# Performance work log

Hardware: AMD Instinct MI355X
Metric: run time of the kernel (lower is better)

The kernel has to match this reference:

```python
import jax, jax.numpy as jnp
import numpy as np

N, E, IN, H, OUT = 100000, 600000, 128, 128, 64
BN_EPS = 1e-5


def setup_inputs() -> dict:
    key = jax.random.key(0)
    ks = jax.random.split(key, 8)
    def lin(k, i, o):
        return jax.random.normal(k, (i, o), jnp.float32) / np.float32(np.sqrt(i))
    return {
        "x": jax.random.normal(ks[0], (N, IN), jnp.float32),
        "edge_index": jax.random.randint(ks[1], (2, E), 0, N, dtype=jnp.int64),
        "W1": lin(ks[2], IN, H), "b1": jnp.zeros((H,), jnp.float32),
        "gamma": jnp.ones((H,), jnp.float32), "beta": jnp.zeros((H,), jnp.float32),
        "W2": lin(ks[3], H, H), "b2": jnp.zeros((H,), jnp.float32),
        "Wm1": lin(ks[4], H, H), "bm1": jnp.zeros((H,), jnp.float32),
        "Wm2": lin(ks[5], H, OUT), "bm2": jnp.zeros((OUT,), jnp.float32),
    }


def reference(x, edge_index, W1, b1, gamma, beta, W2, b2, Wm1, bm1, Wm2, bm2):
    # GINConv: h = MLP((1 + eps) * x + sum_{j in N(i)} x_j), eps = 0 (train_eps=False)
    src = edge_index[0]
    dst = edge_index[1]  # PyG aggregates messages at edge_index[1]
    agg = jax.ops.segment_sum(x[src], dst, num_segments=x.shape[0])  # [N, IN]
    h = agg + x
    # inner MLP: Linear -> BatchNorm (batch stats) -> ReLU -> Linear
    h = h @ W1 + b1
    mean = jnp.mean(h, axis=0)
    var = jnp.var(h, axis=0)
    h = (h - mean) * jax.lax.rsqrt(var + BN_EPS) * gamma + beta
    h = jax.nn.relu(h)
    h = h @ W2 + b2
    h = jax.nn.relu(h)  # .relu() after conv
    # output MLP (norm=None, dropout=0.5 -> identity at inference): Linear -> ReLU -> Linear
    h = jax.nn.relu(h @ Wm1 + bm1)
    return h @ Wm2 + bm2
```

## Files before the change

### kernel.cpp

```cpp
#include <hip/hip_runtime.h>
#include <hip/hip_bf16.h>
#include <stdint.h>

#define NNODES 100000
#define NEDGES 600000
#define SCAN_CHUNK 1024
#define SCAN_NB 98

typedef __attribute__((ext_vector_type(8))) short bf16x8;
typedef __attribute__((ext_vector_type(4))) float f32x4;
typedef __attribute__((ext_vector_type(4))) unsigned int u32x4;

__device__ inline float b2f(short b) {
    union { unsigned u; float f; } v;
    v.u = ((unsigned)(unsigned short)b) << 16;
    return v.f;
}
__device__ inline short f2b(float f) {
    union { float f; unsigned u; } v;
    v.f = f;
    unsigned r = (v.u + 0x7FFFu + ((v.u >> 16) & 1u)) >> 16;
    return (short)r;
}
__device__ inline unsigned packbf(float lo, float hi) {
    return ((unsigned)(unsigned short)f2b(hi) << 16) | (unsigned)(unsigned short)f2b(lo);
}
#define MFMA16(a, b, c) __builtin_amdgcn_mfma_f32_16x16x32_bf16(a, b, c, 0, 0, 0)

__global__ __launch_bounds__(256) void k_prep(const float* __restrict__ x,
                                              const float* __restrict__ W1,
                                              const float* __restrict__ W2,
                                              const float* __restrict__ Wm1,
                                              const float* __restrict__ Wm2,
                                              short* __restrict__ xb, short* __restrict__ Wt,
                                              int* __restrict__ pos, float* __restrict__ stats) {
    int i = blockIdx.x * 256 + threadIdx.x;
    if (i < (NNODES + 1) * 16) {
        bf16x8 o = (bf16x8){0, 0, 0, 0, 0, 0, 0, 0};
        if (i < NNODES * 16) {
            const float4* p = (const float4*)(x + (size_t)i * 8);
            float4 a = p[0], b = p[1];
            o[0] = f2b(a.x); o[1] = f2b(a.y); o[2] = f2b(a.z); o[3] = f2b(a.w);
            o[4] = f2b(b.x); o[5] = f2b(b.y); o[6] = f2b(b.z); o[7] = f2b(b.w);
        }
        *(bf16x8*)(xb + (size_t)i * 8) = o;
    }
    if (i < NNODES) pos[i] = 0;
    if (i < 57344) {
        int jj, lane, kt, ct;
        const float* W;
        int ldw, off;
        if (i < 16384) { off = i; W = W1; ldw = 128; }
        else if (i < 32768) { off = i - 16384; W = W2; ldw = 128; }
        else if (i < 49152) { off = i - 32768; W = Wm1; ldw = 128; }
        else { off = i - 49152; W = Wm2; ldw = 64; }
        jj = off & 7;
        lane = (off >> 3) & 63;
        kt = (off >> 9) & 3;
        ct = (off >> 11) & 7;
        int lr = lane & 15, hi = lane >> 4;
        int c = ct * 16 + lr;
        int k = kt * 32 + hi * 8 + jj;
        Wt[i] = f2b(W[k * ldw + c]);
    }
    if (i < 256) stats[i] = 0.0f;
}


__global__ __launch_bounds__(256) void k_hist(const int* __restrict__ ei, int* __restrict__ cnt) {
    int e = blockIdx.x * 256 + threadIdx.x;
    if (e < NEDGES) atomicAdd(&cnt[ei[NEDGES + e]], 1);
}

__global__ __launch_bounds__(256) void k_scan1(const int* __restrict__ cnt, int* __restrict__ bsums) {
    __shared__ int sd[256];
    int b = blockIdx.x, t = threadIdx.x;
    int base = b * SCAN_CHUNK + t * 4;
    int s = 0;
#pragma unroll
    for (int i = 0; i < 4; ++i) {
        int idx = base + i;
        if (idx < NNODES) s += cnt[idx];
    }
    sd[t] = s;
    __syncthreads();
    for (int off = 128; off > 0; off >>= 1) {
        if (t < off) sd[t] += sd[t + off];
        __syncthreads();
    }
    if (t == 0) bsums[b] = sd[0];
}

__global__ __launch_bounds__(64) void k_scan2(int* __restrict__ bsums, int* __restrict__ rowptr) {
    if (threadIdx.x == 0 && blockIdx.x == 0) {
        int run = 0;
        for (int b = 0; b < SCAN_NB; ++b) {
            int v = bsums[b];
            bsums[b] = run;
            run += v;
        }
        rowptr[NNODES] = run;
    }
}

__global__ __launch_bounds__(256) void k_scan3(const int* __restrict__ cnt,
                                               const int* __restrict__ bsums,
                                               int* __restrict__ rowptr, int* __restrict__ pos) {
    __shared__ int sd[256];
    int b = blockIdx.x, t = threadIdx.x;
    int base = b * SCAN_CHUNK + t * 4;
    int v[4];
    int s = 0;
#pragma unroll
    for (int i = 0; i < 4; ++i) {
        int idx = base + i;
        v[i] = (idx < NNODES) ? cnt[idx] : 0;
        s += v[i];
    }
    sd[t] = s;
    __syncthreads();
    for (int off = 1; off < 256; off <<= 1) {
        int val = (t >= off) ? sd[t - off] : 0;
        __syncthreads();
        sd[t] += val;
        __syncthreads();
    }
    int run = sd[t] - s + bsums[b];
#pragma unroll
    for (int i = 0; i < 4; ++i) {
        int idx = base + i;
        if (idx < NNODES) {
            rowptr[idx] = run;
            pos[idx] = run;
            run += v[i];
        }
    }
}

__global__ __launch_bounds__(256) void k_fill(const int* __restrict__ ei, int* __restrict__ pos,
                                              int* __restrict__ elist) {
    int e = blockIdx.x * 256 + threadIdx.x;
    if (e >= NEDGES) return;
    int src = ei[e];
    int dst = ei[NEDGES + e];
    int p = atomicAdd(&pos[dst], 1);
    elist[p] = src;
}

__global__ __launch_bounds__(256) void k_agg(const short* __restrict__ xb,
                                             const int* __restrict__ rowptr,
                                             const int* __restrict__ elist,
                                             short* __restrict__ bufb) {
    int t = threadIdx.x;
    int w = t >> 6, lane = t & 63;
    int node = blockIdx.x * 4 + w;
    if (node >= NNODES) return;
    int beg = rowptr[node];
    int end = rowptr[node + 1];
    int deg = end - beg;
    int total = deg + 1;
    int sub = lane & 31, half = lane >> 5;
    const uint2* xr = (const uint2*)xb;

    float acc0 = 0.f, acc1 = 0.f, acc2 = 0.f, acc3 = 0.f;

    for (int base = 0; base < total; base += 64) {
        int j = base + lane;
        int ej = NNODES;
        if (j < total) ej = (j == 0) ? node : elist[beg + j - 1];
        int cnt = min(64, total - base);
        int pairs = (cnt + 1) >> 1;
        for (int i = 0; i < pairs; i += 4) {
            int j0 = 2 * i + half;
            int r0 = __shfl(ej, j0);
            int r1 = __shfl(ej, j0 + 2);
            int r2 = __shfl(ej, j0 + 4);
            int r3 = __shfl(ej, j0 + 6);
            uint2 v0 = xr[(size_t)r0 * 32 + sub];
            uint2 v1 = xr[(size_t)r1 * 32 + sub];
            uint2 v2 = xr[(size_t)r2 * 32 + sub];
            uint2 v3 = xr[(size_t)r3 * 32 + sub];
            acc0 += b2f((short)(v0.x & 0xFFFF)) + b2f((short)(v1.x & 0xFFFF)) +
                    b2f((short)(v2.x & 0xFFFF)) + b2f((short)(v3.x & 0xFFFF));
            acc1 += b2f((short)(v0.x >> 16)) + b2f((short)(v1.x >> 16)) +
                    b2f((short)(v2.x >> 16)) + b2f((short)(v3.x >> 16));
            acc2 += b2f((short)(v0.y & 0xFFFF)) + b2f((short)(v1.y & 0xFFFF)) +
                    b2f((short)(v2.y & 0xFFFF)) + b2f((short)(v3.y & 0xFFFF));
            acc3 += b2f((short)(v0.y >> 16)) + b2f((short)(v1.y >> 16)) +
                    b2f((short)(v2.y >> 16)) + b2f((short)(v3.y >> 16));
        }
    }
    acc0 += __shfl_xor(acc0, 32);
    acc1 += __shfl_xor(acc1, 32);
    acc2 += __shfl_xor(acc2, 32);
    acc3 += __shfl_xor(acc3, 32);
    if (half == 0) {
        uint2 o;
        o.x = ((uint32_t)(unsigned short)f2b(acc1) << 16) | (uint32_t)(unsigned short)f2b(acc0);
        o.y = ((uint32_t)(unsigned short)f2b(acc3) << 16) | (uint32_t)(unsigned short)f2b(acc2);
        ((uint2*)bufb)[(size_t)node * 32 + sub] = o;
    }
}

__global__ __launch_bounds__(256) void k_stats(const short* __restrict__ bufb,
                                               const short* __restrict__ W1pk,
                                               float* __restrict__ stats) {
    __shared__ float Sred[2][4][128];
    int t = threadIdx.x, w = t >> 6, l = t & 63;
    int r0 = blockIdx.x * 128;
    int row0 = (w & 1) * 64, col0 = (w >> 1) * 64;

    f32x4 acc[4][4];
#pragma unroll
    for (int r = 0; r < 4; ++r)
#pragma unroll
        for (int c = 0; c < 4; ++c) acc[r][c] = (f32x4){0.f, 0.f, 0.f, 0.f};

#pragma unroll
    for (int kb = 0; kb < 4; ++kb) {
        bf16x8 af[4], bw[4];
#pragma unroll
        for (int r = 0; r < 4; ++r)
            af[r] = *(const bf16x8*)(bufb + (size_t)(r0 + row0 + r * 16 + (l & 15)) * 128 +
                                     kb * 32 + (l >> 4) * 8);
#pragma unroll
        for (int c = 0; c < 4; ++c)
            bw[c] = *(const bf16x8*)(W1pk + ((((w >> 1) * 4 + c) * 4 + kb) * 64 + l) * 8);
#pragma unroll
        for (int r = 0; r < 4; ++r)
#pragma unroll
            for (int c = 0; c < 4; ++c) acc[r][c] = MFMA16(af[r], bw[c], acc[r][c]);
    }

    float s[4], q[4];
#pragma unroll
    for (int c = 0; c < 4; ++c) { s[c] = 0.f; q[c] = 0.f; }
#pragma unroll
    for (int c = 0; c < 4; ++c)
#pragma unroll
        for (int r = 0; r < 4; ++r)
#pragma unroll
            for (int rr = 0; rr < 4; ++rr) {
                int grow = r0 + row0 + r * 16 + (l >> 4) * 4 + rr;
                if (grow < NNODES) {
                    float v = acc[r][c][rr];
                    s[c] += v;
                    q[c] += v * v;
                }
            }
#pragma unroll
    for (int c = 0; c < 4; ++c) {
        s[c] += __shfl_xor(s[c], 16); s[c] += __shfl_xor(s[c], 32);
        q[c] += __shfl_xor(q[c], 16); q[c] += __shfl_xor(q[c], 32);
    }
    if (l < 16) {
#pragma unroll
        for (int c = 0; c < 4; ++c) {
            Sred[0][w][col0 + c * 16 + l] = s[c];
            Sred[1][w][col0 + c * 16 + l] = q[c];
        }
    }
    __syncthreads();
    if (t < 128) {
        int wb = (t < 64) ? 0 : 2;
        atomicAdd(stats + t, Sred[0][wb][t] + Sred[0][wb + 1][t]);
        atomicAdd(stats + 128 + t, Sred[1][wb][t] + Sred[1][wb + 1][t]);
    }
}

__global__ __launch_bounds__(256, 4) void k_mlp(const short* __restrict__ bufb,
                                                const float* __restrict__ stats,
                                                const float* __restrict__ gamma,
                                                const float* __restrict__ beta,
                                                const short* __restrict__ Wt,
                                                const float* __restrict__ b2,
                                                const float* __restrict__ bm1,
                                                const float* __restrict__ bm2,
                                                float* __restrict__ out) {
    __shared__ float scale[128], shift[128], b2s[128], bm1s[128], bm2s[64];

    int t = threadIdx.x, w = t >> 6, l = t & 63;
    int lr = l & 15, hi = l >> 4;
    size_t node0 = (size_t)blockIdx.x * 64 + w * 16;
    const short* W1pk = Wt;
    const short* W2pk = Wt + 16384;
    const short* Wm1pk = Wt + 32768;
    const short* Wm2pk = Wt + 49152;

    if (t < 128) {
        float mean = stats[t] * (1.0f / NNODES);
        float var = stats[128 + t] * (1.0f / NNODES) - mean * mean;
        var = fmaxf(var, 0.0f);
        float inv = rsqrtf(var + 1e-5f);
        float sc = gamma[t] * inv;
        scale[t] = sc;
        shift[t] = beta[t] - mean * sc;
        b2s[t] = b2[t];
        bm1s[t] = bm1[t];
    }
    if (t < 64) bm2s[t] = bm2[t];
    __syncthreads();

    bf16x8 bv[4];
#pragma unroll
    for (int kt = 0; kt < 4; ++kt)
        bv[kt] = *(const bf16x8*)(bufb + (node0 + lr) * 128 + kt * 32 + hi * 8);

    unsigned pw[8][2];

#pragma unroll
    for (int ct = 0; ct < 8; ++ct) {
        f32x4 a = (f32x4){0.f, 0.f, 0.f, 0.f};
#pragma unroll
        for (int kt = 0; kt < 4; ++kt)
            a = MFMA16(*(const bf16x8*)(W1pk + ((ct * 4 + kt) * 64 + l) * 8), bv[kt], a);
        int c0 = ct * 16 + hi * 4;
        float4 sc4 = *(const float4*)&scale[c0];
        float4 sh4 = *(const float4*)&shift[c0];
        float v0 = fmaxf(a[0] * sc4.x + sh4.x, 0.f);
        float v1 = fmaxf(a[1] * sc4.y + sh4.y, 0.f);
        float v2 = fmaxf(a[2] * sc4.z + sh4.z, 0.f);
        float v3 = fmaxf(a[3] * sc4.w + sh4.w, 0.f);
        pw[ct][0] = packbf(v0, v1);
        pw[ct][1] = packbf(v2, v3);
    }

#define REDIST()                                                                        \
    {                                                                                   \
        int h2 = hi >> 1, h1 = hi & 1;                                                  \
        _Pragma("unroll") for (int kt = 0; kt < 4; ++kt) {                              \
            unsigned nw[4];                                                             \
            _Pragma("unroll") for (int jp = 0; jp < 4; ++jp) {                          \
                int srcl = (2 * h1 + (jp >> 1)) * 16 + lr;                              \
                unsigned ve = (unsigned)__shfl((int)pw[2 * kt][jp & 1], srcl);          \
                unsigned vo = (unsigned)__shfl((int)pw[2 * kt + 1][jp & 1], srcl);      \
                nw[jp] = h2 ? vo : ve;                                                  \
            }                                                                           \
            u32x4 uq = (u32x4){nw[0], nw[1], nw[2], nw[3]};                             \
            bv[kt] = __builtin_bit_cast(bf16x8, uq);                                    \
        }                                                                               \
    }
    REDIST();

#pragma unroll
    for (int ct = 0; ct < 8; ++ct) {
        f32x4 a = (f32x4){0.f, 0.f, 0.f, 0.f};
#pragma unroll
        for (int kt = 0; kt < 4; ++kt)
            a = MFMA16(*(const bf16x8*)(W2pk + ((ct * 4 + kt) * 64 + l) * 8), bv[kt], a);
        int c0 = ct * 16 + hi * 4;
        float4 bb = *(const float4*)&b2s[c0];
        float v0 = fmaxf(a[0] + bb.x, 0.f);
        float v1 = fmaxf(a[1] + bb.y, 0.f);
        float v2 = fmaxf(a[2] + bb.z, 0.f);
        float v3 = fmaxf(a[3] + bb.w, 0.f);
        pw[ct][0] = packbf(v0, v1);
        pw[ct][1] = packbf(v2, v3);
    }
    REDIST();

#pragma unroll
    for (int ct = 0; ct < 8; ++ct) {
        f32x4 a = (f32x4){0.f, 0.f, 0.f, 0.f};
#pragma unroll
        for (int kt = 0; kt < 4; ++kt)
            a = MFMA16(*(const bf16x8*)(Wm1pk + ((ct * 4 + kt) * 64 + l) * 8), bv[kt], a);
        int c0 = ct * 16 + hi * 4;
        float4 bb = *(const float4*)&bm1s[c0];
        float v0 = fmaxf(a[0] + bb.x, 0.f);
        float v1 = fmaxf(a[1] + bb.y, 0.f);
        float v2 = fmaxf(a[2] + bb.z, 0.f);
        float v3 = fmaxf(a[3] + bb.w, 0.f);
        pw[ct][0] = packbf(v0, v1);
        pw[ct][1] = packbf(v2, v3);
    }
    REDIST();

#pragma unroll
    for (int ct = 0; ct < 4; ++ct) {
        f32x4 a = (f32x4){0.f, 0.f, 0.f, 0.f};
#pragma unroll
        for (int kt = 0; kt < 4; ++kt)
            a = MFMA16(bv[kt], *(const bf16x8*)(Wm2pk + ((ct * 4 + kt) * 64 + l) * 8), a);
        float bias = bm2s[ct * 16 + lr];
#pragma unroll
        for (int rr = 0; rr < 4; ++rr) {
            size_t grow = node0 + hi * 4 + rr;
            if (grow < NNODES) out[grow * 64 + ct * 16 + lr] = a[rr] + bias;
        }
    }
}

extern "C" void kernel_launch(void* const* d_in, const int* in_sizes, int n_in,
                              void* d_out, int out_size, void* d_ws, size_t ws_size,
                              hipStream_t stream) {
    const float* x     = (const float*)d_in[0];
    const int*   ei    = (const int*)d_in[1];
    const float* W1    = (const float*)d_in[2];
    const float* gamma = (const float*)d_in[4];
    const float* beta  = (const float*)d_in[5];
    const float* W2    = (const float*)d_in[6];
    const float* b2    = (const float*)d_in[7];
    const float* Wm1   = (const float*)d_in[8];
    const float* bm1   = (const float*)d_in[9];
    const float* Wm2   = (const float*)d_in[10];
    const float* bm2   = (const float*)d_in[11];
    float* out = (float*)d_out;

    char* ws = (char*)d_ws;
    short* xb    = (short*)ws;
    short* bufb  = xb + (size_t)(NNODES + 1) * 128;
    short* Wt    = bufb + (size_t)(NNODES + 128) * 128;
    float* stats = (float*)(Wt + 57344);
    int* rowptr  = (int*)(stats + 256);
    int* pos     = rowptr + (NNODES + 1);
    int* elist   = pos + NNODES;
    int* bsums   = elist + NEDGES;

    int gE = (NEDGES + 255) / 256;
    int gPrep = ((NNODES + 1) * 16 + 255) / 256;

    k_prep<<<gPrep, 256, 0, stream>>>(x, W1, W2, Wm1, Wm2, xb, Wt, pos, stats);
    k_hist<<<gE, 256, 0, stream>>>(ei, pos);
    k_scan1<<<SCAN_NB, 256, 0, stream>>>(pos, bsums);
    k_scan2<<<1, 64, 0, stream>>>(bsums, rowptr);
    k_scan3<<<SCAN_NB, 256, 0, stream>>>(pos, bsums, rowptr, pos);
    k_fill<<<gE, 256, 0, stream>>>(ei, pos, elist);
    k_agg<<<(NNODES + 3) / 4, 256, 0, stream>>>(xb, rowptr, elist, bufb);

    int nblkS = (NNODES + 127) / 128;
    k_stats<<<nblkS, 256, 0, stream>>>(bufb, Wt, stats);
    int nblkM = (NNODES + 63) / 64;
    k_mlp<<<nblkM, 256, 0, stream>>>(bufb, stats, gamma, beta, Wt, b2, bm1, bm2, out);
}
```

Before: 190.6 us.

## Process two 16-node tiles per wave in MLP kernel to reuse weight loads

Each wave in k_mlp now handles 32 nodes as two 16-row tiles that share every weight fragment load, halving weight traffic per node. The three hidden layers are folded into one loop with per-layer scale/shift tables, and the block count is halved. Register pressure roughly doubles, so launch bounds drop from 4 to 3 blocks per CU, which reduces occupancy. A non-unrolled layer loop may add indexing overhead.

```diff
diff --git a/kernel.cpp b/kernel.cpp
--- a/kernel.cpp
+++ b/kernel.cpp
@@ -268,7 +268,7 @@
     }
 }
 
-__global__ __launch_bounds__(256, 4) void k_mlp(const short* __restrict__ bufb,
+__global__ __launch_bounds__(256, 3) void k_mlp(const short* __restrict__ bufb,
                                                 const float* __restrict__ stats,
                                                 const float* __restrict__ gamma,
                                                 const float* __restrict__ beta,
@@ -277,116 +277,115 @@
                                                 const float* __restrict__ bm1,
                                                 const float* __restrict__ bm2,
                                                 float* __restrict__ out) {
-    __shared__ float scale[128], shift[128], b2s[128], bm1s[128], bm2s[64];
+    __shared__ float scl[3][128], shf[3][128], bm2s[64];
 
     int t = threadIdx.x, w = t >> 6, l = t & 63;
     int lr = l & 15, hi = l >> 4;
-    size_t node0 = (size_t)blockIdx.x * 64 + w * 16;
-    const short* W1pk = Wt;
-    const short* W2pk = Wt + 16384;
-    const short* Wm1pk = Wt + 32768;
+    size_t node0 = (size_t)blockIdx.x * 128 + w * 32;
     const short* Wm2pk = Wt + 49152;
 
     if (t < 128) {
         float mean = stats[t] * (1.0f / NNODES);
-        float var = stats[128 + t] * (1.0f / NNODES) - mean * mean;
-        var = fmaxf(var, 0.0f);
+        float var = fmaxf(stats[128 + t] * (1.0f / NNODES) - mean * mean, 0.0f);
         float inv = rsqrtf(var + 1e-5f);
         float sc = gamma[t] * inv;
-        scale[t] = sc;
-        shift[t] = beta[t] - mean * sc;
-        b2s[t] = b2[t];
-        bm1s[t] = bm1[t];
+        scl[0][t] = sc;
+        shf[0][t] = beta[t] - mean * sc;
+        scl[1][t] = 1.0f;
+        shf[1][t] = b2[t];
+        scl[2][t] = 1.0f;
+        shf[2][t] = bm1[t];
     }
     if (t < 64) bm2s[t] = bm2[t];
     __syncthreads();
 
-    bf16x8 bv[4];
-#pragma unroll
-    for (int kt = 0; kt < 4; ++kt)
-        bv[kt] = *(const bf16x8*)(bufb + (node0 + lr) * 128 + kt * 32 + hi * 8);
-
-    unsigned pw[8][2];
-
-#pragma unroll
-    for (int ct = 0; ct < 8; ++ct) {
-        f32x4 a = (f32x4){0.f, 0.f, 0.f, 0.f};
-#pragma unroll
-        for (int kt = 0; kt < 4; ++kt)
-            a = MFMA16(*(const bf16x8*)(W1pk + ((ct * 4 + kt) * 64 + l) * 8), bv[kt], a);
-        int c0 = ct * 16 + hi * 4;
-        float4 sc4 = *(const float4*)&scale[c0];
-        float4 sh4 = *(const float4*)&shift[c0];
-        float v0 = fmaxf(a[0] * sc4.x + sh4.x, 0.f);
-        float v1 = fmaxf(a[1] * sc4.y + sh4.y, 0.f);
-        float v2 = fmaxf(a[2] * sc4.z + sh4.z, 0.f);
-        float v3 = fmaxf(a[3] * sc4.w + sh4.w, 0.f);
-        pw[ct][0] = packbf(v0, v1);
-        pw[ct][1] = packbf(v2, v3);
-    }
-
-#define REDIST()                                                                        \
-    {                                                                                   \
-        int h2 = hi >> 1, h1 = hi & 1;                                                  \
-        _Pragma("unroll") for (int kt = 0; kt < 4; ++kt) {                              \
-            unsigned nw[4];                                                             \
-            _Pragma("unroll") for (int jp = 0; jp < 4; ++jp) {                          \
-                int srcl = (2 * h1 + (jp >> 1)) * 16 + lr;                              \
-                unsigned ve = (unsigned)__shfl((int)pw[2 * kt][jp & 1], srcl);          \
-                unsigned vo = (unsigned)__shfl((int)pw[2 * kt + 1][jp & 1], srcl);      \
-                nw[jp] = h2 ? vo : ve;                                                  \
-            }                                                                           \
-            u32x4 uq = (u32x4){nw[0], nw[1], nw[2], nw[3]};                             \
-            bv[kt] = __builtin_bit_cast(bf16x8, uq);                                    \
-        }                                                                               \
-    }
-    REDIST();
-
-#pragma unroll
-    for (int ct = 0; ct < 8; ++ct) {
-        f32x4 a = (f32x4){0.f, 0.f, 0.f, 0.f};
-#pragma unroll
-        for (int kt = 0; kt < 4; ++kt)
-            a = MFMA16(*(const bf16x8*)(W2pk + ((ct * 4 + kt) * 64 + l) * 8), bv[kt], a);
-        int c0 = ct * 16 + hi * 4;
-        float4 bb = *(const float4*)&b2s[c0];
-        float v0 = fmaxf(a[0] + bb.x, 0.f);
-        float v1 = fmaxf(a[1] + bb.y, 0.f);
-        float v2 = fmaxf(a[2] + bb.z, 0.f);
-        float v3 = fmaxf(a[3] + bb.w, 0.f);
-        pw[ct][0] = packbf(v0, v1);
-        pw[ct][1] = packbf(v2, v3);
-    }
-    REDIST();
-
-#pragma unroll
-    for (int ct = 0; ct < 8; ++ct) {
-        f32x4 a = (f32x4){0.f, 0.f, 0.f, 0.f};
-#pragma unroll
-        for (int kt = 0; kt < 4; ++kt)
-            a = MFMA16(*(const bf16x8*)(Wm1pk + ((ct * 4 + kt) * 64 + l) * 8), bv[kt], a);
-        int c0 = ct * 16 + hi * 4;
-        float4 bb = *(const float4*)&bm1s[c0];
-        float v0 = fmaxf(a[0] + bb.x, 0.f);
-        float v1 = fmaxf(a[1] + bb.y, 0.f);
-        float v2 = fmaxf(a[2] + bb.z, 0.f);
-        float v3 = fmaxf(a[3] + bb.w, 0.f);
-        pw[ct][0] = packbf(v0, v1);
-        pw[ct][1] = packbf(v2, v3);
-    }
-    REDIST();
+    bf16x8 bvA[4], bvB[4];
+#pragma unroll
+    for (int kt = 0; kt < 4; ++kt) {
+        bvA[kt] = *(const bf16x8*)(bufb + (node0 + lr) * 128 + kt * 32 + hi * 8);
+        bvB[kt] = *(const bf16x8*)(bufb + (node0 + 16 + lr) * 128 + kt * 32 + hi * 8);
+    }
+
+    unsigned pwA[8][2], pwB[8][2];
+
+    for (int g = 0; g < 3; ++g) {
+        const short* Wg = Wt + g * 16384;
+#pragma unroll
+        for (int ch = 0; ch < 2; ++ch) {
+            f32x4 aA[4], aB[4];
+#pragma unroll
+            for (int cc = 0; cc < 4; ++cc) {
+                aA[cc] = (f32x4){0.f, 0.f, 0.f, 0.f};
+                aB[cc] = (f32x4){0.f, 0.f, 0.f, 0.f};
+            }
+#pragma unroll
+            for (int kt = 0; kt < 4; ++kt) {
+                bf16x8 wv[4];
+#pragma unroll
+                for (int cc = 0; cc < 4; ++cc)
+                    wv[cc] = *(const bf16x8*)(Wg + ((((ch * 4 + cc) * 4) + kt) * 64 + l) * 8);
+#pragma unroll
+                for (int cc = 0; cc < 4; ++cc) {
+                    aA[cc] = MFMA16(wv[cc], bvA[kt], aA[cc]);
+                    aB[cc] = MFMA16(wv[cc], bvB[kt], aB[cc]);
+                }
+            }
+#pragma unroll
+            for (int cc = 0; cc < 4; ++cc) {
+                int ct = ch * 4 + cc;
+                int c0 = ct * 16 + hi * 4;
+                float4 s4 = *(const float4*)&scl[g][c0];
+                float4 h4 = *(const float4*)&shf[g][c0];
+                pwA[ct][0] = packbf(fmaxf(aA[cc][0] * s4.x + h4.x, 0.f),
+                                    fmaxf(aA[cc][1] * s4.y + h4.y, 0.f));
+                pwA[ct][1] = packbf(fmaxf(aA[cc][2] * s4.z + h4.z, 0.f),
+                                    fmaxf(aA[cc][3] * s4.w + h4.w, 0.f));
+                pwB[ct][0] = packbf(fmaxf(aB[cc][0] * s4.x + h4.x, 0.f),
+                                    fmaxf(aB[cc][1] * s4.y + h4.y, 0.f));
+                pwB[ct][1] = packbf(fmaxf(aB[cc][2] * s4.z + h4.z, 0.f),
+                                    fmaxf(aB[cc][3] * s4.w + h4.w, 0.f));
+            }
+        }
+        {
+            int h2 = hi >> 1, h1 = hi & 1;
+#pragma unroll
+            for (int kt = 0; kt < 4; ++kt) {
+                unsigned nwA[4], nwB[4];
+#pragma unroll
+                for (int jp = 0; jp < 4; ++jp) {
+                    int srcl = (2 * h1 + (jp >> 1)) * 16 + lr;
+                    unsigned veA = (unsigned)__shfl((int)pwA[2 * kt][jp & 1], srcl);
+                    unsigned voA = (unsigned)__shfl((int)pwA[2 * kt + 1][jp & 1], srcl);
+                    unsigned veB = (unsigned)__shfl((int)pwB[2 * kt][jp & 1], srcl);
+                    unsigned voB = (unsigned)__shfl((int)pwB[2 * kt + 1][jp & 1], srcl);
+                    nwA[jp] = h2 ? voA : veA;
+                    nwB[jp] = h2 ? voB : veB;
+                }
+                u32x4 uqA = (u32x4){nwA[0], nwA[1], nwA[2], nwA[3]};
+                u32x4 uqB = (u32x4){nwB[0], nwB[1], nwB[2], nwB[3]};
+                bvA[kt] = __builtin_bit_cast(bf16x8, uqA);
+                bvB[kt] = __builtin_bit_cast(bf16x8, uqB);
+            }
+        }
+    }
 
 #pragma unroll
     for (int ct = 0; ct < 4; ++ct) {
-        f32x4 a = (f32x4){0.f, 0.f, 0.f, 0.f};
-#pragma unroll
-        for (int kt = 0; kt < 4; ++kt)
-            a = MFMA16(bv[kt], *(const bf16x8*)(Wm2pk + ((ct * 4 + kt) * 64 + l) * 8), a);
+        f32x4 aA = (f32x4){0.f, 0.f, 0.f, 0.f};
+        f32x4 aB = (f32x4){0.f, 0.f, 0.f, 0.f};
+#pragma unroll
+        for (int kt = 0; kt < 4; ++kt) {
+            bf16x8 wv = *(const bf16x8*)(Wm2pk + ((ct * 4 + kt) * 64 + l) * 8);
+            aA = MFMA16(bvA[kt], wv, aA);
+            aB = MFMA16(bvB[kt], wv, aB);
+        }
         float bias = bm2s[ct * 16 + lr];
 #pragma unroll
         for (int rr = 0; rr < 4; ++rr) {
-            size_t grow = node0 + hi * 4 + rr;
-            if (grow < NNODES) out[grow * 64 + ct * 16 + lr] = a[rr] + bias;
+            size_t growA = node0 + hi * 4 + rr;
+            size_t growB = node0 + 16 + hi * 4 + rr;
+            if (growA < NNODES) out[growA * 64 + ct * 16 + lr] = aA[rr] + bias;
+            if (growB < NNODES) out[growB * 64 + ct * 16 + lr] = aB[rr] + bias;
         }
     }
 }
@@ -430,6 +429,6 @@
 
     int nblkS = (NNODES + 127) / 128;
     k_stats<<<nblkS, 256, 0, stream>>>(bufb, Wt, stats);
-    int nblkM = (NNODES + 63) / 64;
+    int nblkM = (NNODES + 127) / 128;
     k_mlp<<<nblkM, 256, 0, stream>>>(bufb, stats, gamma, beta, Wt, b2, bm1, bm2, out);
 }
```

Result: faster. 172.5 us (-9.5%).
